# Optimization experiments

Measured on AMD Instinct MI355X. Metric: run time of the kernel, lower is better.

The kernel has to match this reference:

```python
import jax, jax.numpy as jnp
import numpy as np

BN_EPS = 1e-5

def setup_inputs() -> dict:
    key = jax.random.key(0)
    ks = jax.random.split(key, 8)
    B, C, O, M, K, NR, NT = 64, 8, 8, 32, 32, 8, 8
    ini = float(np.sqrt(3.0 / O / C))
    def p(k):
        return jax.random.uniform(k, (O, C), jnp.float32, -ini, ini)
    return {
        "A": jax.random.normal(ks[0], (B, C, M, K, NR, NT), jnp.float32),
        "P1": p(ks[1]), "P2": p(ks[2]), "P3": p(ks[3]), "P4": p(ks[4]), "P5": p(ks[5]),
        "Wq": p(ks[6]), "Wk": p(ks[7]),
        "gamma": jnp.ones((O,), jnp.float32),
        "beta": jnp.zeros((O,), jnp.float32),
    }

def reference(A, P1, P2, P3, P4, P5, Wq, Wk, gamma, beta):
    B, C, M, Kd, NR, NT = A.shape
    # Branch 1: per-element channel mix, full tensor
    A1 = jnp.einsum('oc,bcmkrt->bomkrt', P1, A)                    # [B,O,M,K,NR,NT]
    # Branch 2: mean over M (axis 2)
    A2 = jnp.einsum('oc,bckrt->bokrt', P2, A.mean(2))[:, :, None]  # [B,O,1,K,NR,NT]
    # Branch 3: mean over NT (axis 5)
    A3 = jnp.einsum('oc,bcmkr->bomkr', P3, A.mean(5))[..., None]   # [B,O,M,K,NR,1]
    # Branch 4: mean over NR (axis 4)
    A4 = jnp.einsum('oc,bcmkt->bomkt', P4, A.mean(4))[:, :, :, :, None, :]  # [B,O,M,K,1,NT]
    # Attention branch over the K axis, built from mean over NR
    temp = A.mean(4)                                               # [B,C,M,K,NT]
    q = jnp.einsum('oc,bcmkt->bomkt', Wq, temp)
    k = jnp.einsum('oc,bcmkt->bomkt', Wk, temp)
    v = jnp.einsum('oc,bcmkt->bomkt', P5, temp)
    alpha = jnp.tanh(jnp.einsum('bomkt,bomlt->bomkl', q, k) / NT)  # [B,O,M,K,K]
    A5 = (jnp.einsum('bomkl,bomlt->bomkt', alpha, v) / Kd)[:, :, :, :, None, :]
    out = A1 + 0.1 * A2 + 0.1 * A3 + 0.5 * A4 + 2.0 * A5          # [B,O,M,K,NR,NT]
    out = jax.nn.relu(out)
    # BatchNorm1d (training mode, biased var) over all dims except channel O
    mean = out.mean(axis=(0, 2, 3, 4, 5), keepdims=True)
    var = out.var(axis=(0, 2, 3, 4, 5), keepdims=True)
    g = gamma[None, :, None, None, None, None]
    bta = beta[None, :, None, None, None, None]
    return (out - mean) * jax.lax.rsqrt(var + BN_EPS) * g + bta
```

## Files before the change

### kernel.cpp

```cpp
#include <hip/hip_runtime.h>


using u32 = unsigned int;

__device__ __forceinline__ void ld8f(const float* p, float* f) {
  float4 a = *(const float4*)p;
  float4 b = *(const float4*)(p + 4);
  f[0] = a.x; f[1] = a.y; f[2] = a.z; f[3] = a.w;
  f[4] = b.x; f[5] = b.y; f[6] = b.z; f[7] = b.w;
}
__device__ __forceinline__ void st8f(float* p, const float* f) {
  *(float4*)p = make_float4(f[0], f[1], f[2], f[3]);
  *(float4*)(p + 4) = make_float4(f[4], f[5], f[6], f[7]);
}
__device__ __forceinline__ float fast_tanh(float x) {
  float e = __expf(2.0f * x);
  return 1.0f - 2.0f / (e + 1.0f);
}

__global__ void k0_zero(float* __restrict__ stats) {
  if (threadIdx.x < 16) stats[threadIdx.x] = 0.0f;
}

__global__ void k1_meanm(const float* __restrict__ A, float* __restrict__ meanM) {
  const int bc = blockIdx.x;
  const int tid = threadIdx.x;
  const float* base = A + (size_t)bc * 65536 + tid * 8;
  float acc8[8];
#pragma unroll
  for (int t = 0; t < 8; ++t) acc8[t] = 0.0f;
  for (int m = 0; m < 32; ++m) {
    float f[8];
    ld8f(base + m * 2048, f);
#pragma unroll
    for (int t = 0; t < 8; ++t) acc8[t] += f[t];
  }
#pragma unroll
  for (int t = 0; t < 8; ++t) acc8[t] *= (1.0f / 32.0f);
  st8f(meanM + bc * 2048 + tid * 8, acc8);
}

__global__ __launch_bounds__(256, 2) void k2_main(
    const float* __restrict__ A,
    const float* __restrict__ meanM,
    const float* __restrict__ P1,
    const float* __restrict__ P2,
    const float* __restrict__ P3,
    const float* __restrict__ P4,
    const float* __restrict__ P5,
    const float* __restrict__ Wq,
    const float* __restrict__ Wk,
    float* __restrict__ outp,
    float* __restrict__ stats) {
  __shared__ float qb[8 * 260];
  __shared__ float kb[8 * 260];
  __shared__ float vb[8 * 260];
  __shared__ float a5b[8 * 260];
  __shared__ float sred[64];

  const int tid = threadIdx.x;
  const int b = blockIdx.x >> 5;
  const int m = blockIdx.x & 31;
  const int k = tid >> 3;
  const int r = tid & 7;

  float acc[8][8];
  float tr[8][8];
#pragma unroll
  for (int o = 0; o < 8; ++o)
#pragma unroll
    for (int t = 0; t < 8; ++t) acc[o][t] = 0.0f;

#pragma unroll
  for (int c = 0; c < 8; ++c) {
    float ar[8];
    ld8f(A + ((size_t)((b * 8 + c) * 32 + m) * 2048 + tid * 8), ar);
#pragma unroll
    for (int t = 0; t < 8; ++t) {
      float x = ar[t];
      x += __shfl_xor(x, 1, 64);
      x += __shfl_xor(x, 2, 64);
      x += __shfl_xor(x, 4, 64);
      tr[c][t] = x * 0.125f;
    }
    const float mtc = (ar[0] + ar[1] + ar[2] + ar[3] +
                       ar[4] + ar[5] + ar[6] + ar[7]) * 0.125f;
#pragma unroll
    for (int o = 0; o < 8; ++o) {
      const float w1 = P1[o * 8 + c];
      const float w4 = 0.5f * P4[o * 8 + c];
      const float w3 = 0.1f * P3[o * 8 + c];
#pragma unroll
      for (int t = 0; t < 8; ++t)
        acc[o][t] = fmaf(w1, ar[t], fmaf(w4, tr[c][t], fmaf(w3, mtc, acc[o][t])));
    }
  }

#pragma unroll
  for (int c = 0; c < 8; ++c) {
    float m8[8];
    ld8f(meanM + ((b * 8 + c) * 2048 + tid * 8), m8);
#pragma unroll
    for (int o = 0; o < 8; ++o) {
      const float w2 = 0.1f * P2[o * 8 + c];
#pragma unroll
      for (int t = 0; t < 8; ++t) acc[o][t] = fmaf(w2, m8[t], acc[o][t]);
    }
  }

  {
    float qv[8], kv[8], vv[8];
#pragma unroll
    for (int t = 0; t < 8; ++t) { qv[t] = 0.0f; kv[t] = 0.0f; vv[t] = 0.0f; }
#pragma unroll
    for (int c = 0; c < 8; ++c) {
      const float wq = Wq[r * 8 + c];
      const float wk = Wk[r * 8 + c];
      const float wv = P5[r * 8 + c];
#pragma unroll
      for (int t = 0; t < 8; ++t) {
        qv[t] = fmaf(wq, tr[c][t], qv[t]);
        kv[t] = fmaf(wk, tr[c][t], kv[t]);
        vv[t] = fmaf(wv, tr[c][t], vv[t]);
      }
    }
    st8f(&qb[r * 260 + k * 8], qv);
    st8f(&kb[r * 260 + k * 8], kv);
    st8f(&vb[r * 260 + k * 8], vv);
  }
  __syncthreads();

  {
    const int o = tid >> 5;
    const int kq = (tid >> 2) & 7;
    const int lo = tid & 3;
    float qf[4][8];
#pragma unroll
    for (int kl = 0; kl < 4; ++kl)
      ld8f(&qb[o * 260 + (kq * 4 + kl) * 8], qf[kl]);
    float a5p[4][8];
#pragma unroll
    for (int kl = 0; kl < 4; ++kl)
#pragma unroll
      for (int t = 0; t < 8; ++t) a5p[kl][t] = 0.0f;

#pragma unroll
    for (int ll = 0; ll < 8; ++ll) {
      const int l = lo * 8 + ll;
      float krw[8];
      ld8f(&kb[o * 260 + l * 8], krw);
      float al[4];
#pragma unroll
      for (int kl = 0; kl < 4; ++kl) {
        float s = 0.0f;
#pragma unroll
        for (int t = 0; t < 8; ++t) s = fmaf(qf[kl][t], krw[t], s);
        al[kl] = fast_tanh(s * 0.125f);
      }
      float vrw[8];
      ld8f(&vb[o * 260 + l * 8], vrw);
#pragma unroll
      for (int kl = 0; kl < 4; ++kl)
#pragma unroll
        for (int t = 0; t < 8; ++t)
          a5p[kl][t] = fmaf(al[kl], vrw[t], a5p[kl][t]);
    }
#pragma unroll
    for (int kl = 0; kl < 4; ++kl)
#pragma unroll
      for (int t = 0; t < 8; ++t) {
        float x = a5p[kl][t];
        x += __shfl_xor(x, 1, 64);
        x += __shfl_xor(x, 2, 64);
        a5p[kl][t] = x * 0.0625f;
      }
#pragma unroll
    for (int kl = 0; kl < 4; ++kl) {
      const float w0 = lo == 0 ? a5p[kl][0] : lo == 1 ? a5p[kl][2]
                      : lo == 2 ? a5p[kl][4] : a5p[kl][6];
      const float w1 = lo == 0 ? a5p[kl][1] : lo == 1 ? a5p[kl][3]
                      : lo == 2 ? a5p[kl][5] : a5p[kl][7];
      *(float2*)&a5b[o * 260 + (kq * 4 + kl) * 8 + lo * 2] = make_float2(w0, w1);
    }
  }
  __syncthreads();

  float psum[8], psq[8];
#pragma unroll
  for (int o = 0; o < 8; ++o) { psum[o] = 0.0f; psq[o] = 0.0f; }
  const size_t outbase = (size_t)(b * 256 + m) * 2048 + tid * 8;
#pragma unroll
  for (int o = 0; o < 8; ++o) {
    float a5f[8];
    ld8f(&a5b[o * 260 + k * 8], a5f);
    float x8[8];
#pragma unroll
    for (int t = 0; t < 8; ++t) {
      float x = acc[o][t] + a5f[t];
      x = fmaxf(x, 0.0f);
      psum[o] += x;
      psq[o] = fmaf(x, x, psq[o]);
      x8[t] = x;
    }
    st8f(outp + (outbase + o * 65536), x8);
  }
#pragma unroll
  for (int o = 0; o < 8; ++o) {
    float s = psum[o], q = psq[o];
#pragma unroll
    for (int mask = 32; mask >= 1; mask >>= 1) {
      s += __shfl_xor(s, mask, 64);
      q += __shfl_xor(q, mask, 64);
    }
    psum[o] = s; psq[o] = q;
  }
  const int lane = tid & 63;
  const int wid = tid >> 6;
  if (lane == 0) {
#pragma unroll
    for (int o = 0; o < 8; ++o) {
      sred[wid * 16 + o * 2] = psum[o];
      sred[wid * 16 + o * 2 + 1] = psq[o];
    }
  }
  __syncthreads();
  if (tid < 16) {
    float s = sred[tid] + sred[16 + tid] + sred[32 + tid] + sred[48 + tid];
    atomicAdd(&stats[tid], s);
  }
}

__global__ void k3_norm(float* __restrict__ outp,
                        const float* __restrict__ stats,
                        const float* __restrict__ gamma,
                        const float* __restrict__ beta) {
  const int idx = blockIdx.x * 256 + threadIdx.x;
  const size_t e0 = (size_t)idx * 8;
  const int o = (int)(e0 >> 16) & 7;
  const float N = 4194304.0f;
  const float mean = stats[o * 2] / N;
  float var = stats[o * 2 + 1] / N - mean * mean;
  var = fmaxf(var, 0.0f);
  const float inv = rsqrtf(var + 1e-5f);
  const float g = gamma[o] * inv;
  const float sh = beta[o] - mean * g;
  float f[8];
  ld8f(outp + e0, f);
#pragma unroll
  for (int t = 0; t < 8; ++t) f[t] = fmaf(f[t], g, sh);
  st8f(outp + e0, f);
}

extern "C" void kernel_launch(void* const* d_in, const int* in_sizes, int n_in,
                              void* d_out, int out_size, void* d_ws, size_t ws_size,
                              hipStream_t stream) {
  const float* A  = (const float*)d_in[0];
  const float* P1 = (const float*)d_in[1];
  const float* P2 = (const float*)d_in[2];
  const float* P3 = (const float*)d_in[3];
  const float* P4 = (const float*)d_in[4];
  const float* P5 = (const float*)d_in[5];
  const float* Wq = (const float*)d_in[6];
  const float* Wk = (const float*)d_in[7];
  const float* gamma = (const float*)d_in[8];
  const float* beta  = (const float*)d_in[9];
  float* outp = (float*)d_out;

  float* stats = (float*)d_ws;
  float* meanM = (float*)((char*)d_ws + 256);

  hipLaunchKernelGGL(k0_zero, dim3(1), dim3(64), 0, stream, stats);
  hipLaunchKernelGGL(k1_meanm, dim3(512), dim3(256), 0, stream, A, meanM);
  hipLaunchKernelGGL(k2_main, dim3(2048), dim3(256), 0, stream,
                     A, meanM, P1, P2, P3, P4, P5, Wq, Wk, outp, stats);
  hipLaunchKernelGGL(k3_norm, dim3(16384), dim3(256), 0, stream,
                     outp, stats, gamma, beta);
}
```

Measured before the change: 393.3 us.

## Precompute P2 branch, fuse qkv into channel loop, stage intermediate in bf16

The mean-over-M kernel now also applies the P2 channel mix and zeroes the stats, so the separate zero kernel goes away and the main kernel reads 8 precomputed A2 rows instead of 8 meanM rows and doing the mixing itself. The q/k/v projections are folded into the per-channel loop, which drops the 8x8 tr register array, and occupancy hint is raised to 4. When the workspace is large enough, the pre-normalisation activations are written as bf16 to scratch and the norm kernel reads them back, halving intermediate traffic at the cost of bf16 rounding error before batch norm.

```diff
diff --git a/kernel.cpp b/kernel.cpp
--- a/kernel.cpp
+++ b/kernel.cpp
@@ -1,6 +1,7 @@
 #include <hip/hip_runtime.h>
 
 
+using u16 = unsigned short;
 using u32 = unsigned int;
 
 __device__ __forceinline__ void ld8f(const float* p, float* f) {
@@ -13,44 +14,57 @@
   *(float4*)p = make_float4(f[0], f[1], f[2], f[3]);
   *(float4*)(p + 4) = make_float4(f[4], f[5], f[6], f[7]);
 }
+__device__ __forceinline__ u16 f2b(float f) {
+  u32 x = __float_as_uint(f);
+  x += 0x7fffu + ((x >> 16) & 1u);
+  return (u16)(x >> 16);
+}
+__device__ __forceinline__ float b2f(u16 h) {
+  return __uint_as_float(((u32)h) << 16);
+}
 __device__ __forceinline__ float fast_tanh(float x) {
   float e = __expf(2.0f * x);
   return 1.0f - 2.0f / (e + 1.0f);
 }
 
-__global__ void k0_zero(float* __restrict__ stats) {
-  if (threadIdx.x < 16) stats[threadIdx.x] = 0.0f;
-}
-
-__global__ void k1_meanm(const float* __restrict__ A, float* __restrict__ meanM) {
-  const int bc = blockIdx.x;
+__global__ __launch_bounds__(256, 4) void k1_a2pre(
+    const float* __restrict__ A, const float* __restrict__ P2,
+    float* __restrict__ a2pre, float* __restrict__ stats) {
+  const int b = blockIdx.x >> 3;
+  const int kq = blockIdx.x & 7;
   const int tid = threadIdx.x;
-  const float* base = A + (size_t)bc * 65536 + tid * 8;
-  float acc8[8];
-#pragma unroll
-  for (int t = 0; t < 8; ++t) acc8[t] = 0.0f;
-  for (int m = 0; m < 32; ++m) {
-    float f[8];
-    ld8f(base + m * 2048, f);
-#pragma unroll
-    for (int t = 0; t < 8; ++t) acc8[t] += f[t];
-  }
-#pragma unroll
-  for (int t = 0; t < 8; ++t) acc8[t] *= (1.0f / 32.0f);
-  st8f(meanM + bc * 2048 + tid * 8, acc8);
-}
-
-__global__ __launch_bounds__(256, 2) void k2_main(
+  if (blockIdx.x == 0 && tid < 16) stats[tid] = 0.0f;
+  const int j = kq * 256 + tid;
+  float mc[8];
+#pragma unroll
+  for (int c = 0; c < 8; ++c) {
+    const float* base = A + ((size_t)(b * 8 + c) * 65536 + j);
+    float s = 0.0f;
+#pragma unroll
+    for (int m = 0; m < 32; ++m) s += base[m * 2048];
+    mc[c] = s * (1.0f / 32.0f);
+  }
+#pragma unroll
+  for (int o = 0; o < 8; ++o) {
+    float a2 = 0.0f;
+#pragma unroll
+    for (int c = 0; c < 8; ++c) a2 = fmaf(P2[o * 8 + c], mc[c], a2);
+    a2pre[(size_t)(b * 8 + o) * 2048 + j] = 0.1f * a2;
+  }
+}
+
+template <bool BF16OUT>
+__global__ __launch_bounds__(256, 4) void k2_main(
     const float* __restrict__ A,
-    const float* __restrict__ meanM,
+    const float* __restrict__ a2pre,
     const float* __restrict__ P1,
-    const float* __restrict__ P2,
     const float* __restrict__ P3,
     const float* __restrict__ P4,
     const float* __restrict__ P5,
     const float* __restrict__ Wq,
     const float* __restrict__ Wk,
     float* __restrict__ outp,
+    u16* __restrict__ xb,
     float* __restrict__ stats) {
   __shared__ float qb[8 * 260];
   __shared__ float kb[8 * 260];
@@ -65,23 +79,26 @@
   const int r = tid & 7;
 
   float acc[8][8];
-  float tr[8][8];
+  float qv[8], kv[8], vv[8];
 #pragma unroll
   for (int o = 0; o < 8; ++o)
 #pragma unroll
     for (int t = 0; t < 8; ++t) acc[o][t] = 0.0f;
+#pragma unroll
+  for (int t = 0; t < 8; ++t) { qv[t] = 0.0f; kv[t] = 0.0f; vv[t] = 0.0f; }
 
 #pragma unroll
   for (int c = 0; c < 8; ++c) {
     float ar[8];
     ld8f(A + ((size_t)((b * 8 + c) * 32 + m) * 2048 + tid * 8), ar);
+    float trc[8];
 #pragma unroll
     for (int t = 0; t < 8; ++t) {
       float x = ar[t];
       x += __shfl_xor(x, 1, 64);
       x += __shfl_xor(x, 2, 64);
       x += __shfl_xor(x, 4, 64);
-      tr[c][t] = x * 0.125f;
+      trc[t] = x * 0.125f;
     }
     const float mtc = (ar[0] + ar[1] + ar[2] + ar[3] +
                        ar[4] + ar[5] + ar[6] + ar[7]) * 0.125f;
@@ -92,42 +109,30 @@
       const float w3 = 0.1f * P3[o * 8 + c];
 #pragma unroll
       for (int t = 0; t < 8; ++t)
-        acc[o][t] = fmaf(w1, ar[t], fmaf(w4, tr[c][t], fmaf(w3, mtc, acc[o][t])));
-    }
-  }
-
-#pragma unroll
-  for (int c = 0; c < 8; ++c) {
-    float m8[8];
-    ld8f(meanM + ((b * 8 + c) * 2048 + tid * 8), m8);
-#pragma unroll
-    for (int o = 0; o < 8; ++o) {
-      const float w2 = 0.1f * P2[o * 8 + c];
-#pragma unroll
-      for (int t = 0; t < 8; ++t) acc[o][t] = fmaf(w2, m8[t], acc[o][t]);
-    }
-  }
-
-  {
-    float qv[8], kv[8], vv[8];
-#pragma unroll
-    for (int t = 0; t < 8; ++t) { qv[t] = 0.0f; kv[t] = 0.0f; vv[t] = 0.0f; }
-#pragma unroll
-    for (int c = 0; c < 8; ++c) {
-      const float wq = Wq[r * 8 + c];
-      const float wk = Wk[r * 8 + c];
-      const float wv = P5[r * 8 + c];
-#pragma unroll
-      for (int t = 0; t < 8; ++t) {
-        qv[t] = fmaf(wq, tr[c][t], qv[t]);
-        kv[t] = fmaf(wk, tr[c][t], kv[t]);
-        vv[t] = fmaf(wv, tr[c][t], vv[t]);
-      }
-    }
-    st8f(&qb[r * 260 + k * 8], qv);
-    st8f(&kb[r * 260 + k * 8], kv);
-    st8f(&vb[r * 260 + k * 8], vv);
-  }
+        acc[o][t] = fmaf(w1, ar[t], fmaf(w4, trc[t], fmaf(w3, mtc, acc[o][t])));
+    }
+    const float wq = Wq[r * 8 + c];
+    const float wk = Wk[r * 8 + c];
+    const float wv = P5[r * 8 + c];
+#pragma unroll
+    for (int t = 0; t < 8; ++t) {
+      qv[t] = fmaf(wq, trc[t], qv[t]);
+      kv[t] = fmaf(wk, trc[t], kv[t]);
+      vv[t] = fmaf(wv, trc[t], vv[t]);
+    }
+  }
+
+#pragma unroll
+  for (int o = 0; o < 8; ++o) {
+    float a2v[8];
+    ld8f(a2pre + ((size_t)(b * 8 + o) * 2048 + tid * 8), a2v);
+#pragma unroll
+    for (int t = 0; t < 8; ++t) acc[o][t] += a2v[t];
+  }
+
+  st8f(&qb[r * 260 + k * 8], qv);
+  st8f(&kb[r * 260 + k * 8], kv);
+  st8f(&vb[r * 260 + k * 8], vv);
   __syncthreads();
 
   {
@@ -202,7 +207,16 @@
       psq[o] = fmaf(x, x, psq[o]);
       x8[t] = x;
     }
-    st8f(outp + (outbase + o * 65536), x8);
+    if (BF16OUT) {
+      uint4 u;
+      u.x = (u32)f2b(x8[0]) | ((u32)f2b(x8[1]) << 16);
+      u.y = (u32)f2b(x8[2]) | ((u32)f2b(x8[3]) << 16);
+      u.z = (u32)f2b(x8[4]) | ((u32)f2b(x8[5]) << 16);
+      u.w = (u32)f2b(x8[6]) | ((u32)f2b(x8[7]) << 16);
+      *(uint4*)(xb + (outbase + (size_t)o * 65536)) = u;
+    } else {
+      st8f(outp + (outbase + (size_t)o * 65536), x8);
+    }
   }
 #pragma unroll
   for (int o = 0; o < 8; ++o) {
@@ -230,10 +244,10 @@
   }
 }
 
-__global__ void k3_norm(float* __restrict__ outp,
-                        const float* __restrict__ stats,
-                        const float* __restrict__ gamma,
-                        const float* __restrict__ beta) {
+__global__ void k3_norm_inplace(float* __restrict__ outp,
+                                const float* __restrict__ stats,
+                                const float* __restrict__ gamma,
+                                const float* __restrict__ beta) {
   const int idx = blockIdx.x * 256 + threadIdx.x;
   const size_t e0 = (size_t)idx * 8;
   const int o = (int)(e0 >> 16) & 7;
@@ -246,6 +260,32 @@
   const float sh = beta[o] - mean * g;
   float f[8];
   ld8f(outp + e0, f);
+#pragma unroll
+  for (int t = 0; t < 8; ++t) f[t] = fmaf(f[t], g, sh);
+  st8f(outp + e0, f);
+}
+
+__global__ void k3_norm_bf16(const u16* __restrict__ xb,
+                             float* __restrict__ outp,
+                             const float* __restrict__ stats,
+                             const float* __restrict__ gamma,
+                             const float* __restrict__ beta) {
+  const int idx = blockIdx.x * 256 + threadIdx.x;
+  const size_t e0 = (size_t)idx * 8;
+  const int o = (int)(e0 >> 16) & 7;
+  const float N = 4194304.0f;
+  const float mean = stats[o * 2] / N;
+  float var = stats[o * 2 + 1] / N - mean * mean;
+  var = fmaxf(var, 0.0f);
+  const float inv = rsqrtf(var + 1e-5f);
+  const float g = gamma[o] * inv;
+  const float sh = beta[o] - mean * g;
+  const uint4 u = *(const uint4*)(xb + e0);
+  float f[8];
+  f[0] = b2f((u16)(u.x & 0xffffu)); f[1] = b2f((u16)(u.x >> 16));
+  f[2] = b2f((u16)(u.y & 0xffffu)); f[3] = b2f((u16)(u.y >> 16));
+  f[4] = b2f((u16)(u.z & 0xffffu)); f[5] = b2f((u16)(u.z >> 16));
+  f[6] = b2f((u16)(u.w & 0xffffu)); f[7] = b2f((u16)(u.w >> 16));
 #pragma unroll
   for (int t = 0; t < 8; ++t) f[t] = fmaf(f[t], g, sh);
   st8f(outp + e0, f);
@@ -267,12 +307,21 @@
   float* outp = (float*)d_out;
 
   float* stats = (float*)d_ws;
-  float* meanM = (float*)((char*)d_ws + 256);
-
-  hipLaunchKernelGGL(k0_zero, dim3(1), dim3(64), 0, stream, stats);
-  hipLaunchKernelGGL(k1_meanm, dim3(512), dim3(256), 0, stream, A, meanM);
-  hipLaunchKernelGGL(k2_main, dim3(2048), dim3(256), 0, stream,
-                     A, meanM, P1, P2, P3, P4, P5, Wq, Wk, outp, stats);
-  hipLaunchKernelGGL(k3_norm, dim3(16384), dim3(256), 0, stream,
-                     outp, stats, gamma, beta);
-}
+  float* a2pre = (float*)((char*)d_ws + 256);
+  u16* xb = (u16*)((char*)d_ws + 256 + (size_t)4 * 1024 * 1024);
+  const size_t need_bf16 = 256 + (size_t)4 * 1024 * 1024 + (size_t)67108864;
+  const bool use_bf16 = (ws_size >= need_bf16);
+
+  hipLaunchKernelGGL(k1_a2pre, dim3(512), dim3(256), 0, stream, A, P2, a2pre, stats);
+  if (use_bf16) {
+    hipLaunchKernelGGL((k2_main<true>), dim3(2048), dim3(256), 0, stream,
+                       A, a2pre, P1, P3, P4, P5, Wq, Wk, outp, xb, stats);
+    hipLaunchKernelGGL(k3_norm_bf16, dim3(16384), dim3(256), 0, stream,
+                       xb, outp, stats, gamma, beta);
+  } else {
+    hipLaunchKernelGGL((k2_main<false>), dim3(2048), dim3(256), 0, stream,
+                       A, a2pre, P1, P3, P4, P5, Wq, Wk, outp, xb, stats);
+    hipLaunchKernelGGL(k3_norm_inplace, dim3(16384), dim3(256), 0, stream,
+                       outp, stats, gamma, beta);
+  }
+}
```

New measurement: 694.4 us. 76.6% more time.
